# Optimization experiments

Measured on AMD Instinct MI355X. Metric: run time of the kernel, lower is better.

## Reference

```python
import jax, jax.numpy as jnp
import numpy as np

N_BONES = 8
NV = 14062
PARENTS = [-1, 0, 1, 2, 3, 4, 5, 6]  # kinematic chain


def rotvec_to_rotmat(rv):
    # rv: [..., 3] -> [..., 3, 3] via Rodrigues
    ang = jnp.sqrt(jnp.sum(rv * rv, axis=-1) + 1e-12)  # [...]
    k = rv / ang[..., None]
    kx, ky, kz = k[..., 0], k[..., 1], k[..., 2]
    z = jnp.zeros_like(kx)
    K = jnp.stack([
        jnp.stack([z, -kz, ky], -1),
        jnp.stack([kz, z, -kx], -1),
        jnp.stack([-ky, kx, z], -1)], -2)  # [...,3,3]
    s = jnp.sin(ang)[..., None, None]
    c = jnp.cos(ang)[..., None, None]
    I = jnp.eye(3, dtype=rv.dtype)
    return I + s * K + (1.0 - c) * (K @ K)


def bilinear_sample(img, gx, gy):
    # img: [H, W]; gx, gy: [B, Nv] normalized coords in [-1,1]
    # bilinear, border padding, align_corners=True (matches F.grid_sample)
    H, W = img.shape
    x = jnp.clip((gx + 1.0) * 0.5 * (W - 1), 0.0, W - 1.0)
    y = jnp.clip((gy + 1.0) * 0.5 * (H - 1), 0.0, H - 1.0)
    x0 = jnp.floor(x); y0 = jnp.floor(y)
    x0i = x0.astype(jnp.int32); y0i = y0.astype(jnp.int32)
    x1i = jnp.minimum(x0i + 1, W - 1); y1i = jnp.minimum(y0i + 1, H - 1)
    wx = x - x0; wy = y - y0
    v00 = img[y0i, x0i]; v01 = img[y0i, x1i]
    v10 = img[y1i, x0i]; v11 = img[y1i, x1i]
    return (v00 * (1 - wx) + v01 * wx) * (1 - wy) + (v10 * (1 - wx) + v11 * wx) * wy


def setup_inputs() -> dict:
    key = jax.random.key(0)
    ks = jax.random.split(key, 12)
    B = 256
    theta = jax.random.normal(ks[0], (B, N_BONES, 3), jnp.float32) * 0.3
    tau = jax.random.normal(ks[1], (B, 1), jnp.float32) * 0.1
    alpha = jax.random.uniform(ks[2], (B, 1), jnp.float32)
    bsw = jax.random.uniform(ks[3], (B, 55), jnp.float32)
    W = jax.random.uniform(ks[4], (N_BONES, NV), jnp.float32) + 1e-3
    W = W / W.sum(axis=0, keepdims=True)  # done in HACK.__init__
    T = jax.random.normal(ks[5], (NV, 3), jnp.float32)
    P = jax.random.normal(ks[6], (N_BONES, 3, 3, NV, 3), jnp.float32) * 0.01
    L = jax.random.uniform(ks[7], (1, 1, 256, 256), jnp.float32)
    ts = jax.random.normal(ks[8], (NV, 3), jnp.float32)
    # L2P: per-bone rigid transforms (rotation + small translation)
    rv = jax.random.normal(ks[9], (N_BONES, 3), jnp.float32) * 0.2
    R = rotvec_to_rotmat(rv)
    t = jax.random.normal(ks[10], (N_BONES, 3), jnp.float32) * 0.1
    L2P = jnp.tile(jnp.eye(4, dtype=jnp.float32), (N_BONES, 1, 1))
    L2P = L2P.at[:, :3, :3].set(R).at[:, :3, 3].set(t)
    E = jax.random.normal(ks[11], (55, NV, 3), jnp.float32) * 0.05
    uvgrid = jax.random.uniform(jax.random.fold_in(key, 99), (NV, 2), jnp.float32)
    return {"theta": theta, "tau": tau, "alpha": alpha, "bsw": bsw, "W": W,
            "T": T, "P": P, "L": L, "ts": ts, "L2P": L2P, "E": E, "uvgrid": uvgrid}


def reference(theta, tau, alpha, bsw, W, T, P, L, ts, L2P, E, uvgrid):
    B = theta.shape[0]
    R = rotvec_to_rotmat(theta)  # [B, Nb, 3, 3]
    # theta_matrix_zero: bone 0 subtracts itself (-> 0), others subtract I
    sub = jnp.concatenate([R[:, :1],
                           jnp.broadcast_to(jnp.eye(3, dtype=R.dtype), (B, N_BONES - 1, 3, 3))], axis=1)
    theta_zero = R - sub  # [B, Nb, 3, 3]
    # pose-corrective blendshapes: sum over (bone, i, j)
    P_theta = jnp.einsum('bnij,nijvk->bvk', theta_zero, P)  # [B, Nv, 3]

    # forward kinematics along chain: L2W_pose[i] = L2W_pose[parent] @ (L2P[i] @ local[i])
    local = jnp.tile(jnp.eye(4, dtype=R.dtype), (B, N_BONES, 1, 1))
    local = local.at[:, :, :3, :3].set(R)  # [B, Nb, 4, 4]
    mats = []
    for i in range(N_BONES):
        Ai = jnp.einsum('ij,bjk->bik', L2P[i], local[:, i])
        if PARENTS[i] >= 0:
            Ai = jnp.matmul(mats[PARENTS[i]], Ai)
        mats.append(Ai)
    L2W_pose = jnp.stack(mats, axis=1)  # [B, Nb, 4, 4]

    # rest-pose world-to-local (inverse bind matrices)
    rest = []
    for i in range(N_BONES):
        rest.append(L2P[i] if PARENTS[i] < 0 else rest[PARENTS[i]] @ L2P[i])
    W2L = jnp.linalg.inv(jnp.stack(rest))  # [Nb, 4, 4]

    W2L2pWs = jnp.einsum('bnij,njk->bnik', L2W_pose, W2L)  # [B, Nb, 4, 4]
    # skinning-weight contraction over bones -> per-vertex 4x4 transform
    M = jnp.einsum('bnij,nv->bvij', W2L2pWs, W)  # [B, Nv, 4, 4]

    # larynx displacement via grid_sample
    uv = uvgrid * 2.0 - 1.0  # [Nv, 2]
    gx = jnp.broadcast_to(uv[None, :, 0], (B, uv.shape[0]))
    gy = uv[None, :, 1] + tau * 2.0  # shift y by tau*2 (F.pad(tau*2,[1,0]))
    dist = bilinear_sample(L[0, 0], gx, gy)  # [B, Nv]
    L_tau = dist[:, :, None] * ts[None]  # [B, Nv, 3]

    T_theta = (T[None] + P_theta
               + jnp.einsum('bn,nvk->bvk', bsw, E)
               + L_tau * alpha[:, :, None])  # [B, Nv, 3]

    # homogeneous per-vertex 4x4 matvec, keep xyz
    T_transformed = (jnp.einsum('bvij,bvj->bvi', M[:, :, :3, :3], T_theta)
                     + M[:, :, :3, 3])
    return T_transformed
```

## Files before the change

kernel.cpp:

```cpp
#include <hip/hip_runtime.h>
#include <cmath>

#define NB     8
#define NVERT  14062
#define NV3    42186
#define BATCH  256
#define BBLK   64
#define NBT    16
#define KP     63
#define KE     55
#define KTOT   118
#define VT     64

__device__ inline void mat4mul(const float* A, const float* B, float* C) {
#pragma unroll
  for (int i = 0; i < 4; i++)
#pragma unroll
    for (int j = 0; j < 4; j++) {
      float s = 0.f;
#pragma unroll
      for (int k = 0; k < 4; k++) s = fmaf(A[i*4+k], B[k*4+j], s);
      C[i*4+j] = s;
    }
}

__global__ void setup_kernel(const float* __restrict__ theta,
                             const float* __restrict__ bsw,
                             const float* __restrict__ L2P,
                             float* __restrict__ coef_t,
                             float* __restrict__ mats)
{
  int b = blockIdx.x * blockDim.x + threadIdx.x;
  if (b >= BATCH) return;

  float R[NB][9];
#pragma unroll
  for (int n = 0; n < NB; n++) {
    float rx = theta[(b*NB+n)*3+0];
    float ry = theta[(b*NB+n)*3+1];
    float rz = theta[(b*NB+n)*3+2];
    float ang = sqrtf(rx*rx + ry*ry + rz*rz + 1e-12f);
    float kx = rx/ang, ky = ry/ang, kz = rz/ang;
    float s = sinf(ang), c = cosf(ang);
    float K[9] = {0.f,-kz,ky,  kz,0.f,-kx,  -ky,kx,0.f};
    float K2[9];
#pragma unroll
    for (int i = 0; i < 3; i++)
#pragma unroll
      for (int j = 0; j < 3; j++) {
        float v = 0.f;
#pragma unroll
        for (int k = 0; k < 3; k++) v = fmaf(K[i*3+k], K[k*3+j], v);
        K2[i*3+j] = v;
      }
#pragma unroll
    for (int e = 0; e < 9; e++) {
      int i = e/3, j = e%3;
      R[n][e] = (i==j ? 1.f : 0.f) + s*K[e] + (1.f-c)*K2[e];
    }
  }

#pragma unroll
  for (int n = 1; n < NB; n++)
#pragma unroll
    for (int e = 0; e < 9; e++) {
      int i = e/3, j = e%3;
      coef_t[((n-1)*9+e)*BATCH + b] = R[n][e] - (i==j ? 1.f : 0.f);
    }
  for (int s2 = 0; s2 < KE; s2++)
    coef_t[(KP+s2)*BATCH + b] = bsw[b*KE + s2];

  float prevPose[16], prevRest[16];
#pragma unroll 1
  for (int n = 0; n < NB; n++) {
    float loc[16] = {R[n][0],R[n][1],R[n][2],0.f,
                     R[n][3],R[n][4],R[n][5],0.f,
                     R[n][6],R[n][7],R[n][8],0.f,
                     0.f,0.f,0.f,1.f};
    float A[16], pose[16], rest[16];
    mat4mul(&L2P[n*16], loc, A);
    if (n == 0) {
#pragma unroll
      for (int q = 0; q < 16; q++) { pose[q] = A[q]; rest[q] = L2P[q]; }
    } else {
      mat4mul(prevPose, A, pose);
      mat4mul(prevRest, &L2P[n*16], rest);
    }
    float w2l[16];
#pragma unroll
    for (int i = 0; i < 3; i++) {
#pragma unroll
      for (int j = 0; j < 3; j++) w2l[i*4+j] = rest[j*4+i];
      w2l[i*4+3] = -(rest[0*4+i]*rest[0*4+3] + rest[1*4+i]*rest[1*4+3] + rest[2*4+i]*rest[2*4+3]);
    }
    w2l[12]=0.f; w2l[13]=0.f; w2l[14]=0.f; w2l[15]=1.f;
    float skin[16];
    mat4mul(pose, w2l, skin);
#pragma unroll
    for (int i = 0; i < 3; i++)
#pragma unroll
      for (int j = 0; j < 4; j++)
        mats[(size_t)b*96 + n*12 + i*4 + j] = skin[i*4+j];
#pragma unroll
    for (int q = 0; q < 16; q++) { prevPose[q] = pose[q]; prevRest[q] = rest[q]; }
  }
}

__global__ __launch_bounds__(256) void fused_kernel(
    const float* __restrict__ P, const float* __restrict__ E,
    const float* __restrict__ coef_t, const float* __restrict__ matsg,
    const float* __restrict__ Wm, const float* __restrict__ T,
    const float* __restrict__ ts, const float* __restrict__ uvgrid,
    const float* __restrict__ Limg, const float* __restrict__ tau,
    const float* __restrict__ alpha, float* __restrict__ out)
{
  __shared__ float mlds[BBLK][96];
  __shared__ float ta_s[BBLK], al_s[BBLK];

  int tid  = threadIdx.x;
  int lane = tid & 63;
  int wv   = tid >> 6;
  int bbase = blockIdx.x * BBLK;
  int vbase = blockIdx.y * VT;
  int v = vbase + lane;
  bool vok = v < NVERT;
  int vc = vok ? v : NVERT - 1;
  size_t voff = (size_t)vc * 3;

#pragma unroll
  for (int r = 0; r < 6; r++) {
    int q = tid + r*256;
    int bb = q / 24, chunk = q - bb*24;
    *reinterpret_cast<float4*>(&mlds[bb][chunk*4]) =
        *reinterpret_cast<const float4*>(matsg + (size_t)(bbase+bb)*96 + chunk*4);
  }
  if (tid < BBLK) { ta_s[tid] = tau[bbase+tid]; al_s[tid] = alpha[bbase+tid]; }
  __syncthreads();

  const float* Pb = P + (size_t)9 * NV3;
  const float* cbase = coef_t + bbase + wv*NBT;

  float acc[NBT][3];
#pragma unroll
  for (int j = 0; j < NBT; j++) { acc[j][0]=0.f; acc[j][1]=0.f; acc[j][2]=0.f; }

  float dA0,dA1,dA2, dB0,dB1,dB2;
  float4 cA0,cA1,cA2,cA3, cB0,cB1,cB2,cB3;

  {
    const float* rp = Pb + voff;
    dA0 = rp[0]; dA1 = rp[1]; dA2 = rp[2];
    const float* cp = cbase;
    cA0 = *reinterpret_cast<const float4*>(cp+0);
    cA1 = *reinterpret_cast<const float4*>(cp+4);
    cA2 = *reinterpret_cast<const float4*>(cp+8);
    cA3 = *reinterpret_cast<const float4*>(cp+12);
  }

#define FMA_ROW(D0,D1,D2,C0,C1,C2,C3)                                   \
  {                                                                     \
    float cf[NBT] = {C0.x,C0.y,C0.z,C0.w, C1.x,C1.y,C1.z,C1.w,          \
                     C2.x,C2.y,C2.z,C2.w, C3.x,C3.y,C3.z,C3.w};         \
    _Pragma("unroll")                                                   \
    for (int j = 0; j < NBT; j++) {                                     \
      acc[j][0] = fmaf(cf[j], D0, acc[j][0]);                           \
      acc[j][1] = fmaf(cf[j], D1, acc[j][1]);                           \
      acc[j][2] = fmaf(cf[j], D2, acc[j][2]);                           \
    }                                                                   \
  }

#define LOAD_ROW(cn, D0,D1,D2, C0,C1,C2,C3)                             \
  {                                                                     \
    int c_ = (cn) <= (KTOT-1) ? (cn) : (KTOT-1);                        \
    const float* rp = ((c_ < KP) ? (Pb + (size_t)c_*NV3)                \
                                 : (E + (size_t)(c_-KP)*NV3)) + voff;   \
    D0 = rp[0]; D1 = rp[1]; D2 = rp[2];                                 \
    const float* cp = cbase + (size_t)c_*BATCH;                         \
    C0 = *reinterpret_cast<const float4*>(cp+0);                        \
    C1 = *reinterpret_cast<const float4*>(cp+4);                        \
    C2 = *reinterpret_cast<const float4*>(cp+8);                        \
    C3 = *reinterpret_cast<const float4*>(cp+12);                       \
  }

#pragma unroll 1
  for (int c = 0; c < KTOT; c += 2) {
    LOAD_ROW(c+1, dB0,dB1,dB2, cB0,cB1,cB2,cB3);
    FMA_ROW(dA0,dA1,dA2, cA0,cA1,cA2,cA3);
    LOAD_ROW(c+2, dA0,dA1,dA2, cA0,cA1,cA2,cA3);
    FMA_ROW(dB0,dB1,dB2, cB0,cB1,cB2,cB3);
  }

  float W8[NB];
#pragma unroll
  for (int n = 0; n < NB; n++) W8[n] = Wm[(size_t)n*NVERT + vc];
  float T0 = T[vc*3+0], T1 = T[vc*3+1], T2 = T[vc*3+2];
  float s0 = ts[vc*3+0], s1 = ts[vc*3+1], s2 = ts[vc*3+2];
  float u0 = uvgrid[vc*2+0], u1 = uvgrid[vc*2+1];

  float xc = fminf(fmaxf(u0*255.f, 0.f), 255.f);
  float xf = floorf(xc);
  int x0i = (int)xf;
  int x1i = min(x0i+1, 255);
  float wx = xc - xf;

#pragma unroll
  for (int j = 0; j < NBT; j++) {
    int bl = wv*NBT + j;
    float yc = fminf(fmaxf((u1 + ta_s[bl])*255.f, 0.f), 255.f);
    float yf = floorf(yc);
    int y0i = (int)yf;
    int y1i = min(y0i+1, 255);
    float wy = yc - yf;
    float v00 = Limg[y0i*256 + x0i], v01 = Limg[y0i*256 + x1i];
    float v10 = Limg[y1i*256 + x0i], v11 = Limg[y1i*256 + x1i];
    float dist = (v00*(1.f-wx) + v01*wx)*(1.f-wy) + (v10*(1.f-wx) + v11*wx)*wy;
    float da = dist * al_s[bl];

    float xv0 = acc[j][0] + T0 + da*s0;
    float xv1 = acc[j][1] + T1 + da*s1;
    float xv2 = acc[j][2] + T2 + da*s2;

    float o[3];
#pragma unroll
    for (int i = 0; i < 3; i++) {
      float c0=0.f, c1=0.f, c2=0.f, c3=0.f;
#pragma unroll
      for (int n = 0; n < NB; n++) {
        float4 m = *reinterpret_cast<const float4*>(&mlds[bl][n*12 + i*4]);
        float w = W8[n];
        c0 = fmaf(w, m.x, c0); c1 = fmaf(w, m.y, c1);
        c2 = fmaf(w, m.z, c2); c3 = fmaf(w, m.w, c3);
      }
      o[i] = fmaf(c0, xv0, fmaf(c1, xv1, fmaf(c2, xv2, c3)));
    }
    if (vok) {
      size_t off = (size_t)(bbase + bl)*NV3 + (size_t)v*3;
      out[off+0] = o[0];
      out[off+1] = o[1];
      out[off+2] = o[2];
    }
  }
}

extern "C" void kernel_launch(void* const* d_in, const int* in_sizes, int n_in,
                              void* d_out, int out_size, void* d_ws, size_t ws_size,
                              hipStream_t stream)
{
  const float* theta  = (const float*)d_in[0];
  const float* tau    = (const float*)d_in[1];
  const float* alpha  = (const float*)d_in[2];
  const float* bsw    = (const float*)d_in[3];
  const float* Wm     = (const float*)d_in[4];
  const float* T      = (const float*)d_in[5];
  const float* P      = (const float*)d_in[6];
  const float* L      = (const float*)d_in[7];
  const float* ts     = (const float*)d_in[8];
  const float* L2P    = (const float*)d_in[9];
  const float* E      = (const float*)d_in[10];
  const float* uvgrid = (const float*)d_in[11];
  float* out = (float*)d_out;

  float* coef_t = (float*)d_ws;
  float* mats   = coef_t + (size_t)KTOT * BATCH;

  setup_kernel<<<dim3(4), dim3(64), 0, stream>>>(theta, bsw, L2P, coef_t, mats);
  fused_kernel<<<dim3(BATCH/BBLK, (NVERT + VT - 1) / VT), dim3(256), 0, stream>>>(
      P, E, coef_t, mats, Wm, T, ts, uvgrid, L, tau, alpha, out);
}
```

Measured before the change: 214.4 us.

## Halve batch tile, swizzle block order, triple-buffer coefficient loads with zero-padded K

The per-block batch tile shrinks from 64 to 32, so each wave holds 8 batch accumulators instead of 16. This cuts register pressure and doubles the number of blocks. The grid becomes 1D with a swizzled mapping that groups 8 batch tiles over 8 vertex tiles, so blocks sharing the same P/E rows run close together in time for L2 reuse. The K loop now keeps three rows in flight instead of two, and coef_t is zero-padded to 128 rows so the loop can run to 120 without clamping. The trade-off is that each P/E row is re-read across twice as many batch tiles, and blocks past the vertex range exit early.

```diff
diff --git a/kernel.cpp b/kernel.cpp
--- a/kernel.cpp
+++ b/kernel.cpp
@@ -5,11 +5,13 @@
 #define NVERT  14062
 #define NV3    42186
 #define BATCH  256
-#define BBLK   64
-#define NBT    16
+#define BBLK   32
+#define NBT    8
 #define KP     63
 #define KE     55
 #define KTOT   118
+#define KPAD   120
+#define KALLOC 128
 #define VT     64
 
 __device__ inline void mat4mul(const float* A, const float* B, float* C) {
@@ -69,6 +71,8 @@
     }
   for (int s2 = 0; s2 < KE; s2++)
     coef_t[(KP+s2)*BATCH + b] = bsw[b*KE + s2];
+  for (int r = KTOT; r < KALLOC; r++)
+    coef_t[(size_t)r*BATCH + b] = 0.f;
 
   float prevPose[16], prevRest[16];
 #pragma unroll 1
@@ -114,21 +118,26 @@
     const float* __restrict__ Limg, const float* __restrict__ tau,
     const float* __restrict__ alpha, float* __restrict__ out)
 {
+  int bid = blockIdx.x;
+  int x  = (bid >> 3) & 7;
+  int y  = ((bid >> 6) << 3) | (bid & 7);
+  if (y >= (NVERT + VT - 1) / VT) return;
+
   __shared__ float mlds[BBLK][96];
   __shared__ float ta_s[BBLK], al_s[BBLK];
 
   int tid  = threadIdx.x;
   int lane = tid & 63;
   int wv   = tid >> 6;
-  int bbase = blockIdx.x * BBLK;
-  int vbase = blockIdx.y * VT;
+  int bbase = x * BBLK;
+  int vbase = y * VT;
   int v = vbase + lane;
   bool vok = v < NVERT;
   int vc = vok ? v : NVERT - 1;
-  size_t voff = (size_t)vc * 3;
-
-#pragma unroll
-  for (int r = 0; r < 6; r++) {
+  int voffi = vc * 3;
+
+#pragma unroll
+  for (int r = 0; r < 3; r++) {
     int q = tid + r*256;
     int bb = q / 24, chunk = q - bb*24;
     *reinterpret_cast<float4*>(&mlds[bb][chunk*4]) =
@@ -144,50 +153,40 @@
 #pragma unroll
   for (int j = 0; j < NBT; j++) { acc[j][0]=0.f; acc[j][1]=0.f; acc[j][2]=0.f; }
 
-  float dA0,dA1,dA2, dB0,dB1,dB2;
-  float4 cA0,cA1,cA2,cA3, cB0,cB1,cB2,cB3;
-
-  {
-    const float* rp = Pb + voff;
-    dA0 = rp[0]; dA1 = rp[1]; dA2 = rp[2];
-    const float* cp = cbase;
-    cA0 = *reinterpret_cast<const float4*>(cp+0);
-    cA1 = *reinterpret_cast<const float4*>(cp+4);
-    cA2 = *reinterpret_cast<const float4*>(cp+8);
-    cA3 = *reinterpret_cast<const float4*>(cp+12);
-  }
-
-#define FMA_ROW(D0,D1,D2,C0,C1,C2,C3)                                   \
-  {                                                                     \
-    float cf[NBT] = {C0.x,C0.y,C0.z,C0.w, C1.x,C1.y,C1.z,C1.w,          \
-                     C2.x,C2.y,C2.z,C2.w, C3.x,C3.y,C3.z,C3.w};         \
-    _Pragma("unroll")                                                   \
-    for (int j = 0; j < NBT; j++) {                                     \
-      acc[j][0] = fmaf(cf[j], D0, acc[j][0]);                           \
-      acc[j][1] = fmaf(cf[j], D1, acc[j][1]);                           \
-      acc[j][2] = fmaf(cf[j], D2, acc[j][2]);                           \
-    }                                                                   \
-  }
-
-#define LOAD_ROW(cn, D0,D1,D2, C0,C1,C2,C3)                             \
-  {                                                                     \
-    int c_ = (cn) <= (KTOT-1) ? (cn) : (KTOT-1);                        \
-    const float* rp = ((c_ < KP) ? (Pb + (size_t)c_*NV3)                \
-                                 : (E + (size_t)(c_-KP)*NV3)) + voff;   \
-    D0 = rp[0]; D1 = rp[1]; D2 = rp[2];                                 \
-    const float* cp = cbase + (size_t)c_*BATCH;                         \
-    C0 = *reinterpret_cast<const float4*>(cp+0);                        \
-    C1 = *reinterpret_cast<const float4*>(cp+4);                        \
-    C2 = *reinterpret_cast<const float4*>(cp+8);                        \
-    C3 = *reinterpret_cast<const float4*>(cp+12);                       \
-  }
+  float dA0,dA1,dA2, dB0,dB1,dB2, dC0,dC1,dC2;
+  float4 cA0,cA1, cB0,cB1, cC0,cC1;
+
+#define LOAD_ROW(cn, D0,D1,D2, C0,C1)                                    \
+  {                                                                      \
+    int cd = (cn) <= (KTOT-1) ? (cn) : (KTOT-1);                         \
+    const float* rp = (cd < KP) ? (Pb + (size_t)cd*NV3)                  \
+                                : (E + (size_t)(cd-KP)*NV3);             \
+    D0 = rp[voffi+0]; D1 = rp[voffi+1]; D2 = rp[voffi+2];                \
+    const float* cp = cbase + (size_t)(cn)*BATCH;                        \
+    C0 = *reinterpret_cast<const float4*>(cp+0);                         \
+    C1 = *reinterpret_cast<const float4*>(cp+4);                         \
+  }
+
+#define FMA_ROW(D0,D1,D2, C0,C1)                                         \
+  {                                                                      \
+    float cf[NBT] = {C0.x,C0.y,C0.z,C0.w, C1.x,C1.y,C1.z,C1.w};          \
+    _Pragma("unroll")                                                    \
+    for (int j = 0; j < NBT; j++) {                                      \
+      acc[j][0] = fmaf(cf[j], D0, acc[j][0]);                            \
+      acc[j][1] = fmaf(cf[j], D1, acc[j][1]);                            \
+      acc[j][2] = fmaf(cf[j], D2, acc[j][2]);                            \
+    }                                                                    \
+  }
+
+  LOAD_ROW(0, dA0,dA1,dA2, cA0,cA1);
+  LOAD_ROW(1, dB0,dB1,dB2, cB0,cB1);
+  LOAD_ROW(2, dC0,dC1,dC2, cC0,cC1);
 
 #pragma unroll 1
-  for (int c = 0; c < KTOT; c += 2) {
-    LOAD_ROW(c+1, dB0,dB1,dB2, cB0,cB1,cB2,cB3);
-    FMA_ROW(dA0,dA1,dA2, cA0,cA1,cA2,cA3);
-    LOAD_ROW(c+2, dA0,dA1,dA2, cA0,cA1,cA2,cA3);
-    FMA_ROW(dB0,dB1,dB2, cB0,cB1,cB2,cB3);
+  for (int c = 0; c < KPAD; c += 3) {
+    FMA_ROW(dA0,dA1,dA2, cA0,cA1);  LOAD_ROW(c+3, dA0,dA1,dA2, cA0,cA1);
+    FMA_ROW(dB0,dB1,dB2, cB0,cB1);  LOAD_ROW(c+4, dB0,dB1,dB2, cB0,cB1);
+    FMA_ROW(dC0,dC1,dC2, cC0,cC1);  LOAD_ROW(c+5, dC0,dC1,dC2, cC0,cC1);
   }
 
   float W8[NB];
@@ -261,9 +260,9 @@
   float* out = (float*)d_out;
 
   float* coef_t = (float*)d_ws;
-  float* mats   = coef_t + (size_t)KTOT * BATCH;
+  float* mats   = coef_t + (size_t)KALLOC * BATCH;
 
   setup_kernel<<<dim3(4), dim3(64), 0, stream>>>(theta, bsw, L2P, coef_t, mats);
-  fused_kernel<<<dim3(BATCH/BBLK, (NVERT + VT - 1) / VT), dim3(256), 0, stream>>>(
+  fused_kernel<<<dim3(1792), dim3(256), 0, stream>>>(
       P, E, coef_t, mats, Wm, T, ts, uvgrid, L, tau, alpha, out);
 }
```

After: 216.2 us. No clear change (+0.8%).
